# Kernel optimization log

Hardware: AMD Instinct MI355X
Metric: run time of the kernel (lower is better)

## Reference

```python
import jax, jax.numpy as jnp
import numpy as np
import math

S, B, D, H = 2048, 2, 1024, 16
DK = D // H

def setup_inputs() -> dict:
    key = jax.random.key(0)
    ks = jax.random.split(key, 32)
    f = lambda k, shape, s=1.0: jax.random.normal(k, shape, dtype=jnp.float32) * s
    inp = {
        'qx': f(ks[0], (S, B, D)),
        'kx': f(ks[1], (S, B, D)),
        'vx': f(ks[2], (S, B, D)),
        'qc': f(ks[3], (S, B, D)),
        'kc': f(ks[4], (S, B, D)),
    }
    w = 1.0 / math.sqrt(D)
    names = ['qx_lin', 'kx_lin', 'vx_lin', 'qc_lin', 'kc_lin', 'out_lin']
    for i, n in enumerate(names):
        inp['W_' + n] = f(ks[5 + 2 * i], (D, D), w)
        inp['b_' + n] = f(ks[6 + 2 * i], (D,), w)
    vnames = ['Vqx', 'Vqc', 'Vkx', 'Vkc']
    for i, n in enumerate(vnames):
        inp['W_' + n] = f(ks[17 + 2 * i], (D, 1), w)
        inp['b_' + n] = f(ks[18 + 2 * i], (1,), w)
    return inp

def _forward(qx, kx, vx, qc, kc,
             W_qx_lin, b_qx_lin, W_kx_lin, b_kx_lin, W_vx_lin, b_vx_lin,
             W_qc_lin, b_qc_lin, W_kc_lin, b_kc_lin, W_out_lin, b_out_lin,
             W_Vqx, b_Vqx, W_Vqc, b_Vqc, W_Vkx, b_Vkx, W_Vkc, b_Vkc):
    # [S,B,D] -> [B,S,D]
    qx = jnp.swapaxes(qx, 0, 1)
    kx = jnp.swapaxes(kx, 0, 1)
    vx = jnp.swapaxes(vx, 0, 1)
    qc = jnp.swapaxes(qc, 0, 1)
    kc = jnp.swapaxes(kc, 0, 1)
    bs = qx.shape[0]

    qx = qx @ W_qx_lin + b_qx_lin
    kx = kx @ W_kx_lin + b_kx_lin
    v = vx @ W_vx_lin + b_vx_lin
    qc = qc @ W_qc_lin + b_qc_lin
    kc = kc @ W_kc_lin + b_kc_lin

    lam_q = jax.nn.sigmoid((qx @ W_Vqx + b_Vqx) + (qc @ W_Vqc + b_Vqc))  # [B,S,1]
    lam_k = jax.nn.sigmoid((kx @ W_Vkx + b_Vkx) + (kc @ W_Vkc + b_Vkc))
    q = (1.0 - lam_q) * qx + lam_q * qc
    k = (1.0 - lam_k) * kx + lam_k * kc

    # [B,S,D] -> [B,H,S,dk]
    q = q.reshape(bs, -1, H, DK).transpose(0, 2, 1, 3)
    k = k.reshape(bs, -1, H, DK).transpose(0, 2, 1, 3)
    v = v.reshape(bs, -1, H, DK).transpose(0, 2, 1, 3)

    scores = jnp.einsum('bhqd,bhkd->bhqk', q, k) / math.sqrt(DK)
    attn = jax.nn.softmax(scores, axis=-1)  # dropout is identity in eval
    ctx = jnp.einsum('bhqk,bhkd->bhqd', attn, v)

    concat = ctx.transpose(0, 2, 1, 3).reshape(bs, -1, D)
    out = concat @ W_out_lin + b_out_lin
    return jnp.swapaxes(out, 0, 1)  # back to [S,B,D]

def reference(qx, kx, vx, qc, kc,
              W_qx_lin, b_qx_lin, W_kx_lin, b_kx_lin, W_vx_lin, b_vx_lin,
              W_qc_lin, b_qc_lin, W_kc_lin, b_kc_lin, W_out_lin, b_out_lin,
              W_Vqx, b_Vqx, W_Vqc, b_Vqc, W_Vkx, b_Vkx, W_Vkc, b_Vkc):
    return _forward(qx, kx, vx, qc, kc,
                    W_qx_lin, b_qx_lin, W_kx_lin, b_kx_lin, W_vx_lin, b_vx_lin,
                    W_qc_lin, b_qc_lin, W_kc_lin, b_kc_lin, W_out_lin, b_out_lin,
                    W_Vqx, b_Vqx, W_Vqc, b_Vqc, W_Vkx, b_Vkx, W_Vkc, b_Vkc)
```

## Files before the change

### kernel.cpp

```cpp
#include <hip/hip_runtime.h>
#include <math.h>

typedef unsigned short u16;
typedef __attribute__((ext_vector_type(8))) short short8;
typedef __attribute__((ext_vector_type(4))) float floatx4;
typedef __attribute__((ext_vector_type(4))) unsigned short ushort4v;

__device__ __forceinline__ u16 f2bf(float f) {
    union { float f; unsigned int u; } v; v.f = f;
    unsigned int r = v.u + 0x7fffu + ((v.u >> 16) & 1u);
    return (u16)(r >> 16);
}
__device__ __forceinline__ unsigned int pk2bf(float a, float b) {
#if __has_builtin(__builtin_amdgcn_cvt_pk_bf16_f32)
    auto r = __builtin_amdgcn_cvt_pk_bf16_f32(a, b);
    union { decltype(r) v; unsigned int u; } cv; cv.v = r; return cv.u;
#else
    return (unsigned int)f2bf(a) | ((unsigned int)f2bf(b) << 16);
#endif
}
__device__ __forceinline__ float fexp2(float x) {
#if __has_builtin(__builtin_amdgcn_exp2f)
    return __builtin_amdgcn_exp2f(x);
#else
    return exp2f(x);
#endif
}

__device__ __forceinline__ void swap32(unsigned int& x0, unsigned int& x1, int lane) {
#if __has_builtin(__builtin_amdgcn_permlane32_swap)
    (void)lane;
    auto r = __builtin_amdgcn_permlane32_swap((int)x0, (int)x1, false, false);
    x0 = (unsigned int)r[0]; x1 = (unsigned int)r[1];
#else
    const bool hi = (lane & 32) != 0;
    const unsigned int s = hi ? x0 : x1;
    const unsigned int rr = (unsigned int)__shfl_xor((int)s, 32, 64);
    const unsigned int n0 = hi ? rr : x0;
    const unsigned int n1 = hi ? x1 : rr;
    x0 = n0; x1 = n1;
#endif
}
__device__ __forceinline__ void swap16(unsigned int& x0, unsigned int& x1, int lane) {
#if __has_builtin(__builtin_amdgcn_permlane16_swap)
    (void)lane;
    auto r = __builtin_amdgcn_permlane16_swap((int)x0, (int)x1, false, false);
    x0 = (unsigned int)r[0]; x1 = (unsigned int)r[1];
#else
    const bool hi = (lane & 16) != 0;
    const unsigned int s = hi ? x0 : x1;
    const unsigned int rr = (unsigned int)__shfl_xor((int)s, 16, 64);
    const unsigned int n0 = hi ? rr : x0;
    const unsigned int n1 = hi ? x1 : rr;
    x0 = n0; x1 = n1;
#endif
}

__device__ __forceinline__ void g2l16(const u16* g, u16* l) {
    __builtin_amdgcn_global_load_lds(
        (const __attribute__((address_space(1))) void*)g,
        (__attribute__((address_space(3))) void*)l, 16, 0, 0);
}

struct WFuseJobs { const float* W[4]; const float* wv[4]; const float* bl[4];
                   float* out[4]; float* bdot; };

__global__ __launch_bounds__(256) void wfuse(WFuseJobs wf) {
    const int z = blockIdx.y;
    const float* W = wf.W[z];
    const float* wv = wf.wv[z];
    float* out = wf.out[z];
    const int t = threadIdx.x;
    const int lane = t & 63, w = t >> 6;
#pragma unroll
    for (int i = 0; i < 4; i++) {
        const int row = blockIdx.x * 16 + w * 4 + i;
        const float* Wr = W + (size_t)row * 1024 + lane * 16;
        const float* vr = wv + lane * 16;
        float p = 0.f;
#pragma unroll
        for (int c = 0; c < 4; c++) {
            const floatx4 a = *(const floatx4*)(Wr + c * 4);
            const floatx4 b = *(const floatx4*)(vr + c * 4);
            p += a[0] * b[0] + a[1] * b[1] + a[2] * b[2] + a[3] * b[3];
        }
#pragma unroll
        for (int m = 1; m <= 32; m <<= 1) p += __shfl_xor(p, m);
        if (lane == 0) out[row] = p;
    }
    if (blockIdx.x == 0) {
        const floatx4 bb = *(const floatx4*)(wf.bl[z] + t * 4);
        const floatx4 vv = *(const floatx4*)(wv + t * 4);
        float p = bb[0] * vv[0] + bb[1] * vv[1] + bb[2] * vv[2] + bb[3] * vv[3];
#pragma unroll
        for (int m = 1; m <= 32; m <<= 1) p += __shfl_xor(p, m);
        __shared__ float red[4];
        if ((t & 63) == 0) red[t >> 6] = p;
        __syncthreads();
        if (t == 0) wf.bdot[z] = red[0] + red[1] + red[2] + red[3];
    }
}

struct GCWJobs {
    const float* xa[3]; const float* xc[3];
    const float* w1[3]; const float* w2[3];
    const float* bdot;
    const float* sA[3]; const float* sB[3];
    float* lamout[3];
    u16* dst[3];
    const float* wsrc[6]; u16* wdst[6]; int wstride[6]; int wkoff[6];
};

__global__ __launch_bounds__(256) void gatewt(GCWJobs gj) {
    __shared__ float tile[32][33];
    const int z = blockIdx.y;
    const int t = threadIdx.x;

    if (z >= 3) {
        const int j = z - 3;
        const float* W = gj.wsrc[j];
        u16* Wt = gj.wdst[j];
        const int stride = gj.wstride[j], koff = gj.wkoff[j];
        const int n0 = (blockIdx.x & 31) * 32, k0 = (blockIdx.x >> 5) * 32;
        const int tx = t & 31, ty = t >> 5;
#pragma unroll
        for (int i = 0; i < 4; i++)
            tile[ty + i * 8][tx] = W[(size_t)(k0 + ty + i * 8) * 1024 + n0 + tx];
        __syncthreads();
#pragma unroll
        for (int i = 0; i < 4; i++)
            Wt[(size_t)(n0 + ty + i * 8) * stride + koff + k0 + tx] = f2bf(tile[tx][ty + i * 8]);
        return;
    }

    const int lane = t & 63, w = t >> 6;
    const int row = blockIdx.x * 4 + w;
    const int e0 = lane * 4;

    if (z == 2) {
#pragma unroll
        for (int c = 0; c < 4; c++) {
            const floatx4 a = *(const floatx4*)(gj.xa[2] + (size_t)row * 1024 + c * 256 + e0);
            ushort4v o;
            const unsigned int lo = pk2bf(a[0], a[1]);
            const unsigned int hi = pk2bf(a[2], a[3]);
            o[0] = (u16)(lo & 0xffff); o[1] = (u16)(lo >> 16);
            o[2] = (u16)(hi & 0xffff); o[3] = (u16)(hi >> 16);
            *(ushort4v*)(gj.dst[2] + (size_t)row * 1024 + c * 256 + e0) = o;
        }
        return;
    }

    floatx4 av[4], cv[4];
    float p = 0.f;
#pragma unroll
    for (int c = 0; c < 4; c++) {
        av[c] = *(const floatx4*)(gj.xa[z] + (size_t)row * 1024 + c * 256 + e0);
        cv[c] = *(const floatx4*)(gj.xc[z] + (size_t)row * 1024 + c * 256 + e0);
        const floatx4 w1 = *(const floatx4*)(gj.w1[z] + c * 256 + e0);
        const floatx4 w2 = *(const floatx4*)(gj.w2[z] + c * 256 + e0);
#pragma unroll
        for (int j = 0; j < 4; j++) p += av[c][j] * w1[j] + cv[c][j] * w2[j];
    }
#pragma unroll
    for (int m = 1; m <= 32; m <<= 1) p += __shfl_xor(p, m);
    const float x = p + gj.bdot[2 * z] + gj.bdot[2 * z + 1]
                  + gj.sA[z][0] + gj.sB[z][0];
    const float lam = 1.f / (1.f + exp2f(-x * 1.44269504f));
    if (lane == 0) gj.lamout[z][row] = lam;
    const float oml = 1.f - lam;

    u16* d = gj.dst[z] + (size_t)row * 2048;
#pragma unroll
    for (int c = 0; c < 4; c++) {
        ushort4v o1, o2;
        {
            const unsigned int lo = pk2bf(oml * av[c][0], oml * av[c][1]);
            const unsigned int hi = pk2bf(oml * av[c][2], oml * av[c][3]);
            o1[0] = (u16)(lo & 0xffff); o1[1] = (u16)(lo >> 16);
            o1[2] = (u16)(hi & 0xffff); o1[3] = (u16)(hi >> 16);
        }
        {
            const unsigned int lo = pk2bf(lam * cv[c][0], lam * cv[c][1]);
            const unsigned int hi = pk2bf(lam * cv[c][2], lam * cv[c][3]);
            o2[0] = (u16)(lo & 0xffff); o2[1] = (u16)(lo >> 16);
            o2[2] = (u16)(hi & 0xffff); o2[3] = (u16)(hi >> 16);
        }
        *(ushort4v*)(d + c * 256 + e0) = o1;
        *(ushort4v*)(d + 1024 + c * 256 + e0) = o2;
    }
}

__global__ __launch_bounds__(256) void vtrans(const u16* __restrict__ V,
                                              u16* __restrict__ Vtg) {
    __shared__ u16 tile[32][34];
    const int bh = blockIdx.z, b = bh >> 4, h = bh & 15;
    const int base = b * 1024 + h * 64;
    const int s0 = blockIdx.x * 32, d0 = blockIdx.y * 32;
    const int tx = threadIdx.x & 31, ty = threadIdx.x >> 5;
#pragma unroll
    for (int i = 0; i < 4; i++)
        tile[ty + i * 8][tx] = V[(size_t)(s0 + ty + i * 8) * 2048 + base + d0 + tx];
    __syncthreads();
#pragma unroll
    for (int i = 0; i < 4; i++)
        Vtg[((size_t)bh * 64 + d0 + ty + i * 8) * 2048 + s0 + tx] = tile[tx][ty + i * 8];
}

struct PJob {
    const u16* A; const u16* Bt; int K;
    const float* biasA; const float* biasC; const float* lam;
    u16* out; float* outf; float scale;
};
struct PJobs { PJob j[4]; };

__global__ __launch_bounds__(256, 3) void projall(PJobs jobs) {
    __shared__ __align__(16) u16 As[2][128 * 32];
    __shared__ __align__(16) u16 Bs[2][128 * 32];
    const int nj = gridDim.z;
    const int bid = blockIdx.x + 8 * (blockIdx.y + 32 * blockIdx.z);
    const int sw = (bid & 7) * (32 * nj) + (bid >> 3);
    const PJob jb = jobs.j[sw >> 8];
    const int K = jb.K;
    const int m0 = ((sw >> 3) & 31) * 128;
    const int n0 = (sw & 7) * 128;
    const int t = threadIdx.x;
    const int lane = t & 63;
    const int wid = t >> 6;
    const int wm = wid >> 1, wn = wid & 1;
    const int qd = lane >> 4, lm = lane & 15;

    const floatx4 zero4 = {0.f, 0.f, 0.f, 0.f};
    floatx4 acc[4][4];
#pragma unroll
    for (int i = 0; i < 4; i++)
#pragma unroll
        for (int j2 = 0; j2 < 4; j2++) acc[i][j2] = zero4;

    const int srow = t >> 2;
    const int su = (t & 3) ^ (srow & 3);
    const u16* Ap = jb.A + (size_t)(m0 + srow) * K + su * 8;
    const u16* Bp = jb.Bt + (size_t)(n0 + srow) * K + su * 8;

#define PSTAGE(BUF, KOFF) do {                                         \
        g2l16(Ap + (KOFF),                   &As[BUF][t * 8]);         \
        g2l16(Ap + (KOFF) + (size_t)64 * K,  &As[BUF][2048 + t * 8]);  \
        g2l16(Bp + (KOFF),                   &Bs[BUF][t * 8]);         \
        g2l16(Bp + (KOFF) + (size_t)64 * K,  &Bs[BUF][2048 + t * 8]);  \
    } while (0)

    PSTAGE(0, 0);
    __syncthreads();
    int cur = 0;
    const int ua = (qd ^ (lm & 3)) << 3;
    for (int k0 = 0; k0 < K; k0 += 32) {
        if (k0 + 32 < K) PSTAGE(cur ^ 1, k0 + 32);

        short8 af[4], bfg[4];
#pragma unroll
        for (int i = 0; i < 4; i++) {
            af[i]  = *(const short8*)&As[cur][(wm * 64 + i * 16 + lm) * 32 + ua];
            bfg[i] = *(const short8*)&Bs[cur][(wn * 64 + i * 16 + lm) * 32 + ua];
        }
#pragma unroll
        for (int i = 0; i < 4; i++)
#pragma unroll
            for (int j2 = 0; j2 < 4; j2++)
                acc[i][j2] = __builtin_amdgcn_mfma_f32_16x16x32_bf16(af[i], bfg[j2], acc[i][j2], 0, 0, 0);

        __syncthreads();
        cur ^= 1;
    }
#undef PSTAGE

#pragma unroll
    for (int i = 0; i < 4; i++) {
        const int mb = m0 + wm * 64 + i * 16 + qd * 4;
        float lamv[4];
        if (jb.lam) {
#pragma unroll
            for (int r = 0; r < 4; r++) lamv[r] = jb.lam[mb + r];
        }
#pragma unroll
        for (int j2 = 0; j2 < 4; j2++) {
            const int col = n0 + wn * 64 + j2 * 16 + lm;
            const float bA = jb.biasA[col];
            if (jb.outf) {
#pragma unroll
                for (int r = 0; r < 4; r++)
                    jb.outf[(size_t)(mb + r) * 1024 + col] = acc[i][j2][r] + bA;
            } else if (jb.lam) {
                const float dB = jb.biasC[col] - bA;
#pragma unroll
                for (int r = 0; r < 4; r++)
                    jb.out[(size_t)(mb + r) * 1024 + col] =
                        f2bf((acc[i][j2][r] + bA + lamv[r] * dB) * jb.scale);
            } else {
#pragma unroll
                for (int r = 0; r < 4; r++)
                    jb.out[(size_t)(mb + r) * 1024 + col] =
                        f2bf((acc[i][j2][r] + bA) * jb.scale);
            }
        }
    }
}

__global__ __launch_bounds__(256, 2) void projout(const u16* __restrict__ A,
                                                  const u16* __restrict__ Bt,
                                                  const float* __restrict__ bias,
                                                  float* __restrict__ C) {
    __shared__ __align__(16) u16 As[2][128 * 32];
    __shared__ __align__(16) u16 Bs[2][64 * 32];
    const int K = 1024;
    const int bid = blockIdx.x;
    const int sw = (bid & 7) * 64 + (bid >> 3);
    const int m0 = (sw >> 4) * 128;
    const int n0 = (sw & 15) * 64;
    const int t = threadIdx.x;
    const int lane = t & 63;
    const int wid = t >> 6;
    const int wm = wid >> 1, wn = wid & 1;
    const int qd = lane >> 4, lm = lane & 15;

    const floatx4 zero4 = {0.f, 0.f, 0.f, 0.f};
    floatx4 acc[4][2];
#pragma unroll
    for (int i = 0; i < 4; i++)
#pragma unroll
        for (int j2 = 0; j2 < 2; j2++) acc[i][j2] = zero4;

    const int srow = t >> 2;
    const int su = (t & 3) ^ (srow & 3);
    const u16* Ap = A + (size_t)(m0 + srow) * K + su * 8;
    const u16* Bp = Bt + (size_t)(n0 + srow) * K + su * 8;

#define OSTG(BUF, KOFF) do {                                           \
        g2l16(Ap + (KOFF),                   &As[BUF][t * 8]);         \
        g2l16(Ap + (KOFF) + (size_t)64 * K,  &As[BUF][2048 + t * 8]);  \
        g2l16(Bp + (KOFF),                   &Bs[BUF][t * 8]);         \
    } while (0)

    OSTG(0, 0);
    __syncthreads();
    int cur = 0;
    const int ua = (qd ^ (lm & 3)) << 3;
    for (int k0 = 0; k0 < K; k0 += 32) {
        if (k0 + 32 < K) OSTG(cur ^ 1, k0 + 32);

        short8 af[4], bfg[2];
#pragma unroll
        for (int i = 0; i < 4; i++)
            af[i] = *(const short8*)&As[cur][(wm * 64 + i * 16 + lm) * 32 + ua];
#pragma unroll
        for (int j2 = 0; j2 < 2; j2++)
            bfg[j2] = *(const short8*)&Bs[cur][(wn * 32 + j2 * 16 + lm) * 32 + ua];
#pragma unroll
        for (int i = 0; i < 4; i++)
#pragma unroll
            for (int j2 = 0; j2 < 2; j2++)
                acc[i][j2] = __builtin_amdgcn_mfma_f32_16x16x32_bf16(af[i], bfg[j2], acc[i][j2], 0, 0, 0);

        __syncthreads();
        cur ^= 1;
    }
#undef OSTG

#pragma unroll
    for (int i = 0; i < 4; i++) {
        const int mb = m0 + wm * 64 + i * 16 + qd * 4;
#pragma unroll
        for (int j2 = 0; j2 < 2; j2++) {
            const int col = n0 + wn * 32 + j2 * 16 + lm;
            const float bv = bias[col];
#pragma unroll
            for (int r = 0; r < 4; r++)
                C[(size_t)(mb + r) * 1024 + col] = acc[i][j2][r] + bv;
        }
    }
}

__global__ __launch_bounds__(512, 2) void attn8(
    const u16* __restrict__ Q, const u16* __restrict__ Kk,
    const u16* __restrict__ Vtg, u16* __restrict__ ctxbf) {
    __shared__ __align__(16) u16 SB[16384];

    const int bid = blockIdx.x + 16 * blockIdx.y;
    const int sw = (bid & 7) * 64 + (bid >> 3);
    const int qt = sw & 15;
    const int bh = sw >> 4;
    const int b = bh >> 4, h = bh & 15;
    const int hb = b * 1024 + h * 64;

    const int t = threadIdx.x, lane = t & 63, w = t >> 6;
    const int qd = lane >> 4, lm = lane & 15;
    const int q0w = qt * 128 + w * 16;

    short8 qf[2];
    {
        const u16* qr = Q + (size_t)(q0w + lm) * 2048 + hb;
        qf[0] = *(const short8*)(qr + qd * 8);
        qf[1] = *(const short8*)(qr + 32 + qd * 8);
    }

    const floatx4 zero4 = {0.f, 0.f, 0.f, 0.f};
    floatx4 ctx[4];
#pragma unroll
    for (int g = 0; g < 4; g++) ctx[g] = zero4;
    floatx4 accL = zero4;

    union { unsigned int u[4]; short8 s; } ov;
    ov.u[0] = ov.u[1] = ov.u[2] = ov.u[3] = 0x3F803F80u;
    const short8 onesb = ov.s;

    const int rl = t >> 3;
    const int cuz = (t & 7) ^ (rl & 7);
    const u16* kp = Kk + (size_t)rl * 2048 + hb + cuz * 8;
    const u16* vp = Vtg + ((size_t)bh * 64 + rl) * 2048 + cuz * 8;
    u16* kd = &SB[t * 8];
    u16* vd = &SB[4096 + t * 8];

    const int rdA = lm * 64 + ((qd ^ (lm & 7)) << 3);
    const int rdB = rdA ^ 32;

#define STAGE(BUF) do {                                             \
        g2l16(kp, kd + (BUF) * 8192);                               \
        g2l16(vp, vd + (BUF) * 8192);                               \
        kp += 64 * 2048; vp += 64;                                  \
    } while (0)

#define COMPUTE(BUF) do {                                                          \
        short8 pa[2];                                                              \
        _Pragma("unroll")                                                          \
        for (int gp = 0; gp < 2; gp++) {                                           \
            unsigned int pw[2][2];                                                 \
            _Pragma("unroll")                                                      \
            for (int g0 = 0; g0 < 2; g0++) {                                       \
                const int g = gp * 2 + g0;                                         \
                const short8 kf0 = *(const short8*)&SB[(BUF) * 8192 + g * 1024 + rdA]; \
                const short8 kf1 = *(const short8*)&SB[(BUF) * 8192 + g * 1024 + rdB]; \
                floatx4 st = zero4;                                                \
                st = __builtin_amdgcn_mfma_f32_16x16x32_bf16(kf0, qf[0], st, 0, 0, 0); \
                st = __builtin_amdgcn_mfma_f32_16x16x32_bf16(kf1, qf[1], st, 0, 0, 0); \
                const float e0 = fexp2(st[0]), e1 = fexp2(st[1]);                  \
                const float e2 = fexp2(st[2]), e3 = fexp2(st[3]);                  \
                pw[g0][0] = pk2bf(e0, e1);                                         \
                pw[g0][1] = pk2bf(e2, e3);                                         \
            }                                                                      \
            unsigned int a0 = pw[0][0], b0 = pw[1][0];                             \
            unsigned int a1 = pw[0][1], b1 = pw[1][1];                             \
            swap32(a0, b0, lane); swap32(a1, b1, lane);                            \
            swap16(a0, b0, lane); swap16(a1, b1, lane);                            \
            union { unsigned int u[4]; short8 s; } cvv;                            \
            cvv.u[0] = a0; cvv.u[1] = a1; cvv.u[2] = b0; cvv.u[3] = b1;            \
            pa[gp] = cvv.s;                                                        \
        }                                                                          \
        __builtin_amdgcn_s_setprio(1);                                             \
        _Pragma("unroll")                                                          \
        for (int g = 0; g < 4; g++) {                                              \
            const short8 vb0 = *(const short8*)&SB[(BUF) * 8192 + 4096 + g * 1024 + rdA]; \
            const short8 vb1 = *(const short8*)&SB[(BUF) * 8192 + 4096 + g * 1024 + rdB]; \
            ctx[g] = __builtin_amdgcn_mfma_f32_16x16x32_bf16(pa[0], vb0, ctx[g], 0, 0, 0); \
            ctx[g] = __builtin_amdgcn_mfma_f32_16x16x32_bf16(pa[1], vb1, ctx[g], 0, 0, 0); \
        }                                                                          \
        accL = __builtin_amdgcn_mfma_f32_16x16x32_bf16(pa[0], onesb, accL, 0, 0, 0); \
        accL = __builtin_amdgcn_mfma_f32_16x16x32_bf16(pa[1], onesb, accL, 0, 0, 0); \
        __builtin_amdgcn_s_setprio(0);                                             \
    } while (0)

    STAGE(0);
#pragma unroll 1
    for (int it = 0; it < 16; it++) {
        __syncthreads();
        STAGE(1);
        COMPUTE(0);
        __syncthreads();
        if (it < 15) STAGE(0);
        COMPUTE(1);
    }
#undef STAGE
#undef COMPUTE

#pragma unroll
    for (int r = 0; r < 4; r++) {
        const float inv = 1.0f / accL[r];
        const int srow = q0w + qd * 4 + r;
        u16* orow = ctxbf + (size_t)srow * 2048 + hb;
#pragma unroll
        for (int g = 0; g < 4; g++)
            orow[g * 16 + lm] = f2bf(ctx[g][r] * inv);
    }
}

extern "C" void kernel_launch(void* const* d_in, const int* in_sizes, int n_in,
                              void* d_out, int out_size, void* d_ws, size_t ws_size,
                              hipStream_t stream) {
    const float* qx = (const float*)d_in[0];
    const float* kx = (const float*)d_in[1];
    const float* vx = (const float*)d_in[2];
    const float* qc = (const float*)d_in[3];
    const float* kc = (const float*)d_in[4];
    const float* W_qx = (const float*)d_in[5];   const float* b_qx = (const float*)d_in[6];
    const float* W_kx = (const float*)d_in[7];   const float* b_kx = (const float*)d_in[8];
    const float* W_vx = (const float*)d_in[9];   const float* b_vx = (const float*)d_in[10];
    const float* W_qc = (const float*)d_in[11];  const float* b_qc = (const float*)d_in[12];
    const float* W_kc = (const float*)d_in[13];  const float* b_kc = (const float*)d_in[14];
    const float* W_out = (const float*)d_in[15]; const float* b_out = (const float*)d_in[16];
    const float* W_Vqx = (const float*)d_in[17]; const float* b_Vqx = (const float*)d_in[18];
    const float* W_Vqc = (const float*)d_in[19]; const float* b_Vqc = (const float*)d_in[20];
    const float* W_Vkx = (const float*)d_in[21]; const float* b_Vkx = (const float*)d_in[22];
    const float* W_Vkc = (const float*)d_in[23]; const float* b_Vkc = (const float*)d_in[24];

    char* ws = (char*)d_ws;
    const size_t MB = 1048576;
    u16* Aq  = (u16*)ws;
    u16* Ak  = (u16*)(ws + 16 * MB);
    u16* Av  = (u16*)(ws + 32 * MB);
    u16* Wtq = (u16*)(ws + 40 * MB);
    u16* Wtk = (u16*)(ws + 44 * MB);
    u16* Wtv = (u16*)(ws + 48 * MB);
    u16* Wto = (u16*)(ws + 50 * MB);
    u16* Pv    = (u16*)(ws + 52 * MB);
    u16* qg    = (u16*)(ws + 60 * MB);
    u16* kg    = (u16*)(ws + 68 * MB);
    u16* ctxbf = (u16*)(ws + 76 * MB);
    float* wfused = (float*)(ws + 84 * MB);
    float* bdot   = (float*)(ws + 84 * MB + 16384);
    float* lam    = (float*)(ws + 84 * MB + 16384 + 256);
    u16* Vtg    = (u16*)(ws + 32 * MB);

    WFuseJobs wf;
    wf.W[0] = W_qx; wf.wv[0] = W_Vqx; wf.bl[0] = b_qx; wf.out[0] = wfused;
    wf.W[1] = W_qc; wf.wv[1] = W_Vqc; wf.bl[1] = b_qc; wf.out[1] = wfused + 1024;
    wf.W[2] = W_kx; wf.wv[2] = W_Vkx; wf.bl[2] = b_kx; wf.out[2] = wfused + 2048;
    wf.W[3] = W_kc; wf.wv[3] = W_Vkc; wf.bl[3] = b_kc; wf.out[3] = wfused + 3072;
    wf.bdot = bdot;
    wfuse<<<dim3(64, 4), 256, 0, stream>>>(wf);

    GCWJobs gj;
    gj.xa[0] = qx; gj.xc[0] = qc; gj.w1[0] = wfused;        gj.w2[0] = wfused + 1024;
    gj.sA[0] = b_Vqx; gj.sB[0] = b_Vqc; gj.lamout[0] = lam;        gj.dst[0] = Aq;
    gj.xa[1] = kx; gj.xc[1] = kc; gj.w1[1] = wfused + 2048; gj.w2[1] = wfused + 3072;
    gj.sA[1] = b_Vkx; gj.sB[1] = b_Vkc; gj.lamout[1] = lam + 4096; gj.dst[1] = Ak;
    gj.xa[2] = vx; gj.xc[2] = nullptr; gj.w1[2] = nullptr; gj.w2[2] = nullptr;
    gj.sA[2] = nullptr; gj.sB[2] = nullptr; gj.lamout[2] = nullptr; gj.dst[2] = Av;
    gj.bdot = bdot;
    gj.wsrc[0] = W_qx; gj.wdst[0] = Wtq; gj.wstride[0] = 2048; gj.wkoff[0] = 0;
    gj.wsrc[1] = W_qc; gj.wdst[1] = Wtq; gj.wstride[1] = 2048; gj.wkoff[1] = 1024;
    gj.wsrc[2] = W_kx; gj.wdst[2] = Wtk; gj.wstride[2] = 2048; gj.wkoff[2] = 0;
    gj.wsrc[3] = W_kc; gj.wdst[3] = Wtk; gj.wstride[3] = 2048; gj.wkoff[3] = 1024;
    gj.wsrc[4] = W_vx; gj.wdst[4] = Wtv; gj.wstride[4] = 1024; gj.wkoff[4] = 0;
    gj.wsrc[5] = W_out; gj.wdst[5] = Wto; gj.wstride[5] = 1024; gj.wkoff[5] = 0;
    gatewt<<<dim3(1024, 9), 256, 0, stream>>>(gj);

    const float QSCALE = 0.18033688011112042f;
    PJobs pj;
    pj.j[0].A = Aq; pj.j[0].Bt = Wtq; pj.j[0].K = 2048;
    pj.j[0].biasA = b_qx; pj.j[0].biasC = b_qc; pj.j[0].lam = lam;
    pj.j[0].out = qg; pj.j[0].outf = nullptr; pj.j[0].scale = QSCALE;
    pj.j[1].A = Ak; pj.j[1].Bt = Wtk; pj.j[1].K = 2048;
    pj.j[1].biasA = b_kx; pj.j[1].biasC = b_kc; pj.j[1].lam = lam + 4096;
    pj.j[1].out = kg; pj.j[1].outf = nullptr; pj.j[1].scale = 1.0f;
    pj.j[2].A = Av; pj.j[2].Bt = Wtv; pj.j[2].K = 1024;
    pj.j[2].biasA = b_vx; pj.j[2].biasC = nullptr; pj.j[2].lam = nullptr;
    pj.j[2].out = Pv; pj.j[2].outf = nullptr; pj.j[2].scale = 1.0f;
    pj.j[3] = pj.j[2];
    projall<<<dim3(8, 32, 3), 256, 0, stream>>>(pj);

    vtrans<<<dim3(64, 2, 32), 256, 0, stream>>>(Pv, Vtg);

    attn8<<<dim3(16, 32), 512, 0, stream>>>(qg, kg, Vtg, ctxbf);

    projout<<<dim3(512), 256, 0, stream>>>(ctxbf, Wto, b_out, (float*)d_out);
}
```

Baseline: 322.6 us.

## Rewrite projection GEMM with 256x256 tiles and 4-stage async LDS pipeline

Replaces the 128x128-tile, double-buffered projection kernel with a 512-thread, 256x256-tile kernel. Its k-loop uses four LDS buffers filled by async global-to-LDS loads three stages ahead, gated by explicit vmcnt waits and a single barrier per step. MFMA issue is raised with s_setprio, and the LDS swizzle and block-to-tile mapping are changed to match. The larger tile is meant to cut global and LDS traffic per flop and hide load latency, but it drops the grid to 192 blocks and needs about 128KB of LDS per block, which risks leaving CUs idle at one block per CU.

Result: slower. 349.7 us (+8.4%).

```diff
diff --git a/kernel.cpp b/kernel.cpp
--- a/kernel.cpp
+++ b/kernel.cpp
@@ -214,92 +214,110 @@
 };
 struct PJobs { PJob j[4]; };
 
-__global__ __launch_bounds__(256, 3) void projall(PJobs jobs) {
-    __shared__ __align__(16) u16 As[2][128 * 32];
-    __shared__ __align__(16) u16 Bs[2][128 * 32];
-    const int nj = gridDim.z;
-    const int bid = blockIdx.x + 8 * (blockIdx.y + 32 * blockIdx.z);
-    const int sw = (bid & 7) * (32 * nj) + (bid >> 3);
-    const PJob jb = jobs.j[sw >> 8];
+__global__ __launch_bounds__(512, 2) void proj256p(PJobs jobs) {
+    __shared__ __align__(16) u16 As[4][256 * 32];
+    __shared__ __align__(16) u16 Bs[4][256 * 32];
+
+    const int bid = blockIdx.x + 4 * (blockIdx.y + 16 * blockIdx.z);
+    const int sw = (bid & 7) * 24 + (bid >> 3);
+    const PJob jb = jobs.j[sw >> 6];
+    const int r = sw & 63;
+    const int m0 = (r >> 2) * 256;
+    const int n0 = (r & 3) * 256;
     const int K = jb.K;
-    const int m0 = ((sw >> 3) & 31) * 128;
-    const int n0 = (sw & 7) * 128;
+
     const int t = threadIdx.x;
     const int lane = t & 63;
-    const int wid = t >> 6;
-    const int wm = wid >> 1, wn = wid & 1;
+    const int wv = t >> 6;
+    const int wm = wv >> 2, wn = wv & 3;
     const int qd = lane >> 4, lm = lane & 15;
 
     const floatx4 zero4 = {0.f, 0.f, 0.f, 0.f};
-    floatx4 acc[4][4];
-#pragma unroll
-    for (int i = 0; i < 4; i++)
-#pragma unroll
-        for (int j2 = 0; j2 < 4; j2++) acc[i][j2] = zero4;
+    floatx4 acc[8][4];
+#pragma unroll
+    for (int i = 0; i < 8; i++)
+#pragma unroll
+        for (int j = 0; j < 4; j++) acc[i][j] = zero4;
 
     const int srow = t >> 2;
-    const int su = (t & 3) ^ (srow & 3);
+    const int su = (t & 3) ^ ((t >> 3) & 3);
     const u16* Ap = jb.A + (size_t)(m0 + srow) * K + su * 8;
     const u16* Bp = jb.Bt + (size_t)(n0 + srow) * K + su * 8;
 
-#define PSTAGE(BUF, KOFF) do {                                         \
-        g2l16(Ap + (KOFF),                   &As[BUF][t * 8]);         \
-        g2l16(Ap + (KOFF) + (size_t)64 * K,  &As[BUF][2048 + t * 8]);  \
-        g2l16(Bp + (KOFF),                   &Bs[BUF][t * 8]);         \
-        g2l16(Bp + (KOFF) + (size_t)64 * K,  &Bs[BUF][2048 + t * 8]);  \
+#define STG(BUF, KO) do {                                              \
+        g2l16(Ap + (KO),                   &As[BUF][t * 8]);           \
+        g2l16(Ap + (KO) + (size_t)128 * K, &As[BUF][4096 + t * 8]);    \
+        g2l16(Bp + (KO),                   &Bs[BUF][t * 8]);           \
+        g2l16(Bp + (KO) + (size_t)128 * K, &Bs[BUF][4096 + t * 8]);    \
     } while (0)
 
-    PSTAGE(0, 0);
-    __syncthreads();
-    int cur = 0;
-    const int ua = (qd ^ (lm & 3)) << 3;
-    for (int k0 = 0; k0 < K; k0 += 32) {
-        if (k0 + 32 < K) PSTAGE(cur ^ 1, k0 + 32);
-
-        short8 af[4], bfg[4];
-#pragma unroll
-        for (int i = 0; i < 4; i++) {
-            af[i]  = *(const short8*)&As[cur][(wm * 64 + i * 16 + lm) * 32 + ua];
-            bfg[i] = *(const short8*)&Bs[cur][(wn * 64 + i * 16 + lm) * 32 + ua];
-        }
-#pragma unroll
-        for (int i = 0; i < 4; i++)
-#pragma unroll
-            for (int j2 = 0; j2 < 4; j2++)
-                acc[i][j2] = __builtin_amdgcn_mfma_f32_16x16x32_bf16(af[i], bfg[j2], acc[i][j2], 0, 0, 0);
-
-        __syncthreads();
-        cur ^= 1;
-    }
-#undef PSTAGE
-
-#pragma unroll
-    for (int i = 0; i < 4; i++) {
-        const int mb = m0 + wm * 64 + i * 16 + qd * 4;
+    const int ua = (qd ^ ((lm >> 1) & 3)) << 3;
+    const int aBase = (wm * 128 + lm) * 32 + ua;
+    const int bBase = (wn * 64 + lm) * 32 + ua;
+
+    const int nt = K >> 5;
+    STG(0, 0);
+    STG(1, 32);
+    STG(2, 64);
+
+#pragma unroll 1
+    for (int kt = 0; kt < nt; kt++) {
+        const int rem = nt - 1 - kt;
+        if (rem >= 2)      asm volatile("s_waitcnt vmcnt(8)" ::: "memory");
+        else if (rem == 1) asm volatile("s_waitcnt vmcnt(4)" ::: "memory");
+        else               asm volatile("s_waitcnt vmcnt(0)" ::: "memory");
+        __builtin_amdgcn_s_barrier();
+        if (kt + 3 < nt) {
+            STG((kt + 3) & 3, (kt + 3) * 32);
+        }
+
+        const int buf = kt & 3;
+        const u16* Ab = &As[buf][0];
+        const u16* Bb = &Bs[buf][0];
+
+        short8 bfr[4];
+#pragma unroll
+        for (int j = 0; j < 4; j++)
+            bfr[j] = *(const short8*)&Bb[bBase + j * 16 * 32];
+#pragma unroll
+        for (int i = 0; i < 8; i++) {
+            const short8 af = *(const short8*)&Ab[aBase + i * 16 * 32];
+            __builtin_amdgcn_s_setprio(1);
+#pragma unroll
+            for (int j = 0; j < 4; j++)
+                acc[i][j] = __builtin_amdgcn_mfma_f32_16x16x32_bf16(af, bfr[j], acc[i][j], 0, 0, 0);
+            __builtin_amdgcn_s_setprio(0);
+        }
+    }
+#undef STG
+
+#pragma unroll
+    for (int i = 0; i < 8; i++) {
+        const int mb = m0 + wm * 128 + i * 16 + qd * 4;
         float lamv[4];
         if (jb.lam) {
 #pragma unroll
-            for (int r = 0; r < 4; r++) lamv[r] = jb.lam[mb + r];
-        }
-#pragma unroll
-        for (int j2 = 0; j2 < 4; j2++) {
-            const int col = n0 + wn * 64 + j2 * 16 + lm;
+            for (int rr = 0; rr < 4; rr++) lamv[rr] = jb.lam[mb + rr];
+        }
+#pragma unroll
+        for (int j = 0; j < 4; j++) {
+            const int col = n0 + wn * 64 + j * 16 + lm;
             const float bA = jb.biasA[col];
             if (jb.outf) {
 #pragma unroll
-                for (int r = 0; r < 4; r++)
-                    jb.outf[(size_t)(mb + r) * 1024 + col] = acc[i][j2][r] + bA;
+                for (int rr = 0; rr < 4; rr++)
+                    jb.outf[(size_t)(mb + rr) * 1024 + col] = acc[i][j][rr] + bA;
             } else if (jb.lam) {
                 const float dB = jb.biasC[col] - bA;
 #pragma unroll
-                for (int r = 0; r < 4; r++)
-                    jb.out[(size_t)(mb + r) * 1024 + col] =
-                        f2bf((acc[i][j2][r] + bA + lamv[r] * dB) * jb.scale);
+                for (int rr = 0; rr < 4; rr++)
+                    jb.out[(size_t)(mb + rr) * 1024 + col] =
+                        f2bf((acc[i][j][rr] + bA + lamv[rr] * dB) * jb.scale);
             } else {
 #pragma unroll
-                for (int r = 0; r < 4; r++)
-                    jb.out[(size_t)(mb + r) * 1024 + col] =
-                        f2bf((acc[i][j2][r] + bA) * jb.scale);
+                for (int rr = 0; rr < 4; rr++)
+                    jb.out[(size_t)(mb + rr) * 1024 + col] =
+                        f2bf((acc[i][j][rr] + bA) * jb.scale);
             }
         }
     }
@@ -564,7 +582,7 @@
     pj.j[2].biasA = b_vx; pj.j[2].biasC = nullptr; pj.j[2].lam = nullptr;
     pj.j[2].out = Pv; pj.j[2].outf = nullptr; pj.j[2].scale = 1.0f;
     pj.j[3] = pj.j[2];
-    projall<<<dim3(8, 32, 3), 256, 0, stream>>>(pj);
+    proj256p<<<dim3(4, 16, 3), 512, 0, stream>>>(pj);
 
     vtrans<<<dim3(64, 2, 32), 256, 0, stream>>>(Pv, Vtg);
 
```
